# Optimization experiments

Measured on AMD Instinct MI355X. Metric: run time of the kernel, lower is better.

Reference implementation:

```python
import jax, jax.numpy as jnp
import numpy as np

VOL_RANGE = np.array([-40.0, -40.0, -1.0, 40.0, 40.0, 5.4], dtype=np.float32)
VOXEL = 0.8
NUM_CLASSES = 18
EMPTY_LABEL = NUM_CLASSES - 1
SCALE_MULT = 3.0
N_G = 1024
H, W, D = 100, 100, 8  # (vol_range[3:]-vol_range[:3]) / voxel_size


def quat_to_rotmat(q):
    # q: [N,4] (w,x,y,z), normalized here
    q = q / jnp.linalg.norm(q, axis=-1, keepdims=True)
    w, x, y, z = q[:, 0], q[:, 1], q[:, 2], q[:, 3]
    R = jnp.stack([
        1 - 2 * (y * y + z * z), 2 * (x * y - w * z), 2 * (x * z + w * y),
        2 * (x * y + w * z), 1 - 2 * (x * x + z * z), 2 * (y * z - w * x),
        2 * (x * z - w * y), 2 * (y * z + w * x), 1 - 2 * (x * x + y * y),
    ], axis=-1).reshape(-1, 3, 3)
    return R


def get_covariance(scales, R):
    M = R * scales[:, None, :]          # R @ diag(s)
    return jnp.einsum('nik,njk->nij', M, M)  # M M^T


def grid_points():
    lo = jnp.asarray(VOL_RANGE[:3])
    gx = (jnp.arange(H, dtype=jnp.float32) + 0.5) * VOXEL + lo[0]
    gy = (jnp.arange(W, dtype=jnp.float32) + 0.5) * VOXEL + lo[1]
    gz = (jnp.arange(D, dtype=jnp.float32) + 0.5) * VOXEL + lo[2]
    X, Y, Z = jnp.meshgrid(gx, gy, gz, indexing='ij')
    return jnp.stack([X, Y, Z], axis=-1).reshape(-1, 3)  # [P,3]


def setup_inputs() -> dict:
    key = jax.random.key(0)
    k1, k2, k3, k4, k5 = jax.random.split(key, 5)
    lo, hi = jnp.asarray(VOL_RANGE[:3]), jnp.asarray(VOL_RANGE[3:])
    means3d = jax.random.uniform(k1, (N_G, 3), minval=lo, maxval=hi)
    opacities = jax.random.uniform(k2, (N_G, 1))
    scales = jax.random.uniform(k3, (N_G, 3), minval=0.2, maxval=2.0)
    rotations = jax.random.normal(k4, (N_G, 4))
    features = jax.random.normal(k5, (N_G, NUM_CLASSES - 1))
    empty_scalar = jnp.ones((1,), jnp.float32) * 10.0
    return dict(means3d=means3d, opacities=opacities, scales=scales,
                rotations=rotations, features=features, empty_scalar=empty_scalar)


def reference(means3d, opacities, scales, rotations, features, empty_scalar):
    # covariances from scales + rotations (covariances=None path)
    cov = get_covariance(scales, quat_to_rotmat(rotations))  # [N,3,3]

    # append zero 'empty' channel, then append the empty background gaussian
    feats = jnp.concatenate([features, jnp.zeros_like(features[:, :1])], axis=-1)  # [N,C]
    empty_sem = jnp.zeros((1, NUM_CLASSES), jnp.float32).at[0, EMPTY_LABEL].add(empty_scalar[0])
    feats = jnp.concatenate([feats, empty_sem], axis=0)

    center = jnp.asarray((VOL_RANGE[:3] + VOL_RANGE[3:]) / 2.0)
    rng = jnp.abs(jnp.asarray(VOL_RANGE[:3] - VOL_RANGE[3:]))
    mu = jnp.concatenate([means3d, center[None]], axis=0)                 # [N+1,3]
    cov = jnp.concatenate([cov, jnp.diag(rng ** 2)[None]], axis=0)        # [N+1,3,3]
    opa = jnp.concatenate([opacities[:, 0], jnp.ones((1,))], axis=0)      # [N+1]
    sc = jnp.concatenate([scales, rng[None]], axis=0)                     # [N+1,3]

    x = grid_points()  # [P,3]

    # Mahalanobis distance via quadratic expansion (avoids [P,N,3] residuals):
    A = jnp.linalg.inv(cov)                        # [N+1,3,3]
    B = jnp.einsum('nij,nj->ni', A, mu)            # [N+1,3]
    c = jnp.einsum('ni,ni->n', B, mu)              # [N+1]
    xx = x[:, :, None] * x[:, None, :]             # [P,3,3]
    maha = jnp.einsum('pij,nij->pn', xx, A) - 2.0 * (x @ B.T) + c[None, :]  # [P,N+1]

    # local cutoff: |x - mu| <= scale_multiplier * scale per axis
    r = SCALE_MULT * sc  # [N+1,3]
    mask = jnp.ones((x.shape[0], mu.shape[0]), bool)
    for d in range(3):
        mask &= jnp.abs(x[:, d:d + 1] - mu[None, :, d]) <= r[None, :, d]

    w = jnp.where(mask, opa[None, :] * jnp.exp(-0.5 * maha), 0.0)  # [P,N+1]
    sem = w @ feats                                                # [P,C]

    grid_feats = sem.reshape(H, W, D, NUM_CLASSES)
    grid_density = jnp.zeros((H, W, D, 1), jnp.float32)
    return (grid_density, grid_feats)
```

## Files before the change

### kernel.cpp

```cpp
#include <hip/hip_runtime.h>

#define NG   1024
#define NCLS 18
#define HH   100
#define WW   100
#define DD   8
#define PTOT (HH*WW*DD)
#define TI   2
#define TJ   4
#define CH   64

__global__ __launch_bounds__(64) void gv_fused(
    const float* __restrict__ means, const float* __restrict__ opac,
    const float* __restrict__ scales, const float* __restrict__ rots,
    const float* __restrict__ feats, const float* __restrict__ es,
    float* __restrict__ out)
{
    __shared__ int s_idx[NG];
    __shared__ __align__(16) float s_g[CH][36];

    const int tid = threadIdx.x;
    const int i0  = blockIdx.x * TI;
    const int j0  = blockIdx.y * TJ;

    const float xlo = (i0 + 0.5f) * 0.8f - 40.f;
    const float xhi = (i0 + TI - 0.5f) * 0.8f - 40.f;
    const float ylo = (j0 + 0.5f) * 0.8f - 40.f;
    const float yhi = (j0 + TJ - 0.5f) * 0.8f - 40.f;
    const float zlo = -0.6f, zhi = 5.0f;

    int ns = 0;
    #pragma unroll 4
    for (int it = 0; it < NG / 64; ++it) {
        int n = it * 64 + tid;
        float mx = means[n*3+0], my = means[n*3+1], mz = means[n*3+2];
        float rx = 3.f*scales[n*3+0], ry = 3.f*scales[n*3+1], rz = 3.f*scales[n*3+2];
        bool ov = (mx - rx <= xhi) & (mx + rx >= xlo)
                & (my - ry <= yhi) & (my + ry >= ylo)
                & (mz - rz <= zhi) & (mz + rz >= zlo);
        unsigned long long m = __ballot(ov);
        if (ov) {
            int pos = __popcll(m & ((1ull << tid) - 1ull));
            s_idx[ns + pos] = n;
        }
        ns += (int)__popcll(m);
    }
    __syncthreads();

    const int k = tid & 7, dj = (tid >> 3) & 3, di = tid >> 5;
    const int i = i0 + di, j = j0 + dj;
    const float x = (i + 0.5f) * 0.8f - 40.f;
    const float y = (j + 0.5f) * 0.8f - 40.f;
    const float z = (k + 0.5f) * 0.8f - 1.f;

    float acc[17];
    #pragma unroll
    for (int c = 0; c < 17; ++c) acc[c] = 0.f;

    for (int base = 0; base < ns; base += CH) {
        const int m = min(CH, ns - base);
        __syncthreads();
        if (tid < m) {
            int n = s_idx[base + tid];
            float qw = rots[n*4+0], qx = rots[n*4+1], qy = rots[n*4+2], qz = rots[n*4+3];
            float inv = rsqrtf(qw*qw + qx*qx + qy*qy + qz*qz);
            qw *= inv; qx *= inv; qy *= inv; qz *= inv;
            float R00 = 1.f - 2.f*(qy*qy + qz*qz), R01 = 2.f*(qx*qy - qw*qz), R02 = 2.f*(qx*qz + qw*qy);
            float R10 = 2.f*(qx*qy + qw*qz), R11 = 1.f - 2.f*(qx*qx + qz*qz), R12 = 2.f*(qy*qz - qw*qx);
            float R20 = 2.f*(qx*qz - qw*qy), R21 = 2.f*(qy*qz + qw*qx), R22 = 1.f - 2.f*(qx*qx + qy*qy);
            float sx = scales[n*3+0], sy = scales[n*3+1], sz = scales[n*3+2];
            float ix = 1.f/(sx*sx), iy = 1.f/(sy*sy), iz = 1.f/(sz*sz);
            float* g = s_g[tid];
            g[0] = means[n*3+0]; g[1] = means[n*3+1]; g[2] = means[n*3+2]; g[3] = 3.f*sx;
            g[4] = 3.f*sy; g[5] = 3.f*sz; g[6] = opac[n];
            g[7]  = R00*R00*ix + R01*R01*iy + R02*R02*iz;
            g[8]  = R00*R10*ix + R01*R11*iy + R02*R12*iz;
            g[9]  = R00*R20*ix + R01*R21*iy + R02*R22*iz;
            g[10] = R10*R10*ix + R11*R11*iy + R12*R12*iz;
            g[11] = R10*R20*ix + R11*R21*iy + R12*R22*iz;
            g[12] = R20*R20*ix + R21*R21*iy + R22*R22*iz;
            #pragma unroll
            for (int c = 0; c < 17; ++c) g[13 + c] = feats[n*17 + c];
            g[30] = 0.f; g[31] = 0.f;
        }
        __syncthreads();

        for (int t = 0; t < m; ++t) {
            const float4* gq = (const float4*)s_g[t];
            float4 q0 = gq[0], q1 = gq[1];
            float dx = x - q0.x, dy = y - q0.y, dz = z - q0.z;
            if (fabsf(dx) <= q0.w && fabsf(dy) <= q1.x && fabsf(dz) <= q1.y) {
                float4 q2 = gq[2], q3 = gq[3];
                float maha = dx*(dx*q1.w + 2.f*(dy*q2.x + dz*q2.y))
                           + dy*(dy*q2.z + 2.f*dz*q2.w)
                           + dz*dz*q3.x;
                float w = q1.z * __expf(-0.5f * maha);
                float4 q4 = gq[4], q5 = gq[5], q6 = gq[6], q7 = gq[7];
                acc[0]  = fmaf(w, q3.y, acc[0]);  acc[1]  = fmaf(w, q3.z, acc[1]);
                acc[2]  = fmaf(w, q3.w, acc[2]);
                acc[3]  = fmaf(w, q4.x, acc[3]);  acc[4]  = fmaf(w, q4.y, acc[4]);
                acc[5]  = fmaf(w, q4.z, acc[5]);  acc[6]  = fmaf(w, q4.w, acc[6]);
                acc[7]  = fmaf(w, q5.x, acc[7]);  acc[8]  = fmaf(w, q5.y, acc[8]);
                acc[9]  = fmaf(w, q5.z, acc[9]);  acc[10] = fmaf(w, q5.w, acc[10]);
                acc[11] = fmaf(w, q6.x, acc[11]); acc[12] = fmaf(w, q6.y, acc[12]);
                acc[13] = fmaf(w, q6.z, acc[13]); acc[14] = fmaf(w, q6.w, acc[14]);
                acc[15] = fmaf(w, q7.x, acc[15]); acc[16] = fmaf(w, q7.y, acc[16]);
            }
        }
    }

    const int p = (i * WW + j) * DD + k;
    float dz0 = z - 2.2f;
    float me  = x*x*(1.f/6400.f) + y*y*(1.f/6400.f) + dz0*dz0*(1.f/40.96f);
    float w17 = es[0] * __expf(-0.5f * me);
    out[p] = 0.f;
    float* o = out + PTOT + p * NCLS;
    #pragma unroll
    for (int c = 0; c < 17; ++c) o[c] = acc[c];
    o[17] = w17;
}

extern "C" void kernel_launch(void* const* d_in, const int* in_sizes, int n_in,
                              void* d_out, int out_size, void* d_ws, size_t ws_size,
                              hipStream_t stream) {
    const float* means  = (const float*)d_in[0];
    const float* opac   = (const float*)d_in[1];
    const float* scales = (const float*)d_in[2];
    const float* rots   = (const float*)d_in[3];
    const float* feats  = (const float*)d_in[4];
    const float* es     = (const float*)d_in[5];
    float* out = (float*)d_out;

    dim3 grid(HH / TI, WW / TJ);
    gv_fused<<<grid, 64, 0, stream>>>(means, opac, scales, rots, feats, es, out);
}
```

Measured before the change: 75.25 us.

## Split gaussian loop across thread pairs per voxel and shrink block tile

Each block now covers one x column by 4 y by 8 z voxels, so the grid doubles in x. Two threads share each voxel, each taking alternate gaussians from the chunk, and their partial sums are combined with a cross-lane shuffle. Each thread of the pair writes half of the output channels. The tighter per-block bounding box lets the culling pass keep fewer gaussians per block. In exchange the gaussian list build and the per-gaussian parameter setup now run twice as many times in total.

```diff
diff --git a/kernel.cpp b/kernel.cpp
--- a/kernel.cpp
+++ b/kernel.cpp
@@ -6,7 +6,6 @@
 #define WW   100
 #define DD   8
 #define PTOT (HH*WW*DD)
-#define TI   2
 #define TJ   4
 #define CH   64
 
@@ -20,24 +19,23 @@
     __shared__ __align__(16) float s_g[CH][36];
 
     const int tid = threadIdx.x;
-    const int i0  = blockIdx.x * TI;
+    const int i   = blockIdx.x;
     const int j0  = blockIdx.y * TJ;
 
-    const float xlo = (i0 + 0.5f) * 0.8f - 40.f;
-    const float xhi = (i0 + TI - 0.5f) * 0.8f - 40.f;
-    const float ylo = (j0 + 0.5f) * 0.8f - 40.f;
-    const float yhi = (j0 + TJ - 0.5f) * 0.8f - 40.f;
-    const float zlo = -0.6f, zhi = 5.0f;
+    const float cx = (i + 0.5f) * 0.8f - 40.f;
+    const float cy = (j0 + 2.0f) * 0.8f - 40.f;
+    const float cz = 2.2f;
+    const float hy = 1.2f, hz = 2.8f;
 
     int ns = 0;
     #pragma unroll 4
     for (int it = 0; it < NG / 64; ++it) {
         int n = it * 64 + tid;
         float mx = means[n*3+0], my = means[n*3+1], mz = means[n*3+2];
-        float rx = 3.f*scales[n*3+0], ry = 3.f*scales[n*3+1], rz = 3.f*scales[n*3+2];
-        bool ov = (mx - rx <= xhi) & (mx + rx >= xlo)
-                & (my - ry <= yhi) & (my + ry >= ylo)
-                & (mz - rz <= zhi) & (mz + rz >= zlo);
+        float sx = scales[n*3+0], sy = scales[n*3+1], sz = scales[n*3+2];
+        bool ov = (fabsf(mx - cx) <= 3.f*sx)
+                & (fabsf(my - cy) <= fmaf(3.f, sy, hy))
+                & (fabsf(mz - cz) <= fmaf(3.f, sz, hz));
         unsigned long long m = __ballot(ov);
         if (ov) {
             int pos = __popcll(m & ((1ull << tid) - 1ull));
@@ -47,9 +45,9 @@
     }
     __syncthreads();
 
-    const int k = tid & 7, dj = (tid >> 3) & 3, di = tid >> 5;
-    const int i = i0 + di, j = j0 + dj;
-    const float x = (i + 0.5f) * 0.8f - 40.f;
+    const int vox = tid >> 1, par = tid & 1;
+    const int k = vox & 7, j = j0 + (vox >> 3);
+    const float x = cx;
     const float y = (j + 0.5f) * 0.8f - 40.f;
     const float z = (k + 0.5f) * 0.8f - 1.f;
 
@@ -85,7 +83,7 @@
         }
         __syncthreads();
 
-        for (int t = 0; t < m; ++t) {
+        for (int t = par; t < m; t += 2) {
             const float4* gq = (const float4*)s_g[t];
             float4 q0 = gq[0], q1 = gq[1];
             float dx = x - q0.x, dy = y - q0.y, dz = z - q0.z;
@@ -109,15 +107,23 @@
         }
     }
 
+    #pragma unroll
+    for (int c = 0; c < 17; ++c) acc[c] += __shfl_xor(acc[c], 1, 64);
+
     const int p = (i * WW + j) * DD + k;
     float dz0 = z - 2.2f;
     float me  = x*x*(1.f/6400.f) + y*y*(1.f/6400.f) + dz0*dz0*(1.f/40.96f);
     float w17 = es[0] * __expf(-0.5f * me);
-    out[p] = 0.f;
     float* o = out + PTOT + p * NCLS;
-    #pragma unroll
-    for (int c = 0; c < 17; ++c) o[c] = acc[c];
-    o[17] = w17;
+    if (par == 0) {
+        out[p] = 0.f;
+        #pragma unroll
+        for (int c = 0; c < 9; ++c) o[c] = acc[c];
+    } else {
+        #pragma unroll
+        for (int c = 9; c < 17; ++c) o[c] = acc[c];
+        o[17] = w17;
+    }
 }
 
 extern "C" void kernel_launch(void* const* d_in, const int* in_sizes, int n_in,
@@ -131,6 +137,6 @@
     const float* es     = (const float*)d_in[5];
     float* out = (float*)d_out;
 
-    dim3 grid(HH / TI, WW / TJ);
+    dim3 grid(HH, WW / TJ);
     gv_fused<<<grid, 64, 0, stream>>>(means, opac, scales, rots, feats, es, out);
 }
```

New measurement: 76.21 us. Within noise of the previous version (+1.3%).
